# Kernel tuning notes

Measured on AMD Instinct MI355X. Metric: run time of the kernel, lower is better.

Reference implementation:

```python
import jax, jax.numpy as jnp
import numpy as np

N, M, D, C = 8192, 4096, 512, 100


def mish(x):
    return x * jnp.tanh(jax.nn.softplus(x))


def encode_dml(x, W1, b1, W2, b2):
    # two Linear(d_in, d_in) layers each followed by Mish
    h = mish(x @ W1 + b1)
    return mish(h @ W2 + b2)


def setup_inputs() -> dict:
    key = jax.random.key(0)
    ks = jax.random.split(key, 8)
    s = 1.0 / np.sqrt(D)
    x = jax.random.normal(ks[0], (N, D), dtype=jnp.float32)
    samples = jax.random.normal(ks[1], (M, D), dtype=jnp.float32)
    W1 = jax.random.normal(ks[2], (D, D), dtype=jnp.float32) * s
    b1 = jnp.zeros((D,), dtype=jnp.float32)
    W2 = jax.random.normal(ks[3], (D, D), dtype=jnp.float32) * s
    b2 = jnp.zeros((D,), dtype=jnp.float32)
    Wp = jax.random.normal(ks[4], (M, C), dtype=jnp.float32) * (1.0 / np.sqrt(M))
    bp = jnp.zeros((C,), dtype=jnp.float32)
    return {"x": x, "samples": samples, "W1": W1, "b1": b1,
            "W2": W2, "b2": b2, "Wp": Wp, "bp": bp}


def reference(x, samples, W1, b1, W2, b2, Wp, bp):
    xe = encode_dml(x, W1, b1, W2, b2)        # [N, D]
    se = encode_dml(samples, W1, b1, W2, b2)  # [M, D]
    # Euclidean distance to every anchor, GEMM-trick form of
    # torch.norm(x[:,None,:] - s[None,:,:], dim=-1)
    d2 = (jnp.sum(xe * xe, axis=1)[:, None]
          + jnp.sum(se * se, axis=1)[None, :]
          - 2.0 * (xe @ se.T))                # [N, M]
    dist = jnp.sqrt(jnp.maximum(d2, 0.0))
    z = jnp.tanh(dist @ Wp + bp)              # [N, C]
    return jax.nn.log_softmax(z, axis=1)
```

## Files before the change

### kernel.cpp

```cpp
#include <hip/hip_runtime.h>
#include <hip/hip_bf16.h>
#include <math.h>

#define N_ 8192
#define M_ 4096
#define R_ 12288
#define D_ 512
#define C_ 100
#define CP_ 112
#define NSPLIT_ 8
#define MTILES_ ((M_ / NSPLIT_) / 128)

typedef _Float16 f16;
typedef f16  f16x8 __attribute__((ext_vector_type(8)));
typedef f16  f16x4 __attribute__((ext_vector_type(4)));
typedef float f32x4 __attribute__((ext_vector_type(4)));

__device__ __forceinline__ float mishf(float v) {
    float sp = fmaxf(v, 0.f) + log1pf(expf(-fabsf(v)));
    return v * tanhf(sp);
}

__global__ void prep_all(const float* __restrict__ W1, const float* __restrict__ W2,
                         const float* __restrict__ Wp,
                         f16* __restrict__ w1t, f16* __restrict__ w2t,
                         f16* __restrict__ wpT, float* __restrict__ n2) {
    __shared__ char pshm[57856];
    const int bid = blockIdx.x, t = threadIdx.x;
    if (bid < 128) {
        float (*ls)[68] = (float (*)[68])pshm;
        const float* W = (bid < 64) ? W1 : W2;
        f16* WT = (bid < 64) ? w1t : w2t;
        int tile = bid & 63;
        int k0 = (tile >> 3) * 64, c0 = (tile & 7) * 64;
        int r = t >> 4, c4 = (t & 15) * 4;
        #pragma unroll
        for (int l = 0; l < 4; ++l) {
            int row = r + 16 * l;
            float4 v = *reinterpret_cast<const float4*>(&W[(size_t)(k0 + row) * D_ + c0 + c4]);
            ls[row][c4 + 0] = v.x; ls[row][c4 + 1] = v.y;
            ls[row][c4 + 2] = v.z; ls[row][c4 + 3] = v.w;
        }
        __syncthreads();
        #pragma unroll
        for (int l = 0; l < 4; ++l) {
            int c = r + 16 * l;
            f16x4 o;
            #pragma unroll
            for (int j = 0; j < 4; ++j) o[j] = (f16)ls[c4 + j][c];
            *reinterpret_cast<f16x4*>(&WT[(size_t)(c0 + c) * D_ + k0 + c4]) = o;
        }
    } else if (bid < 160) {
        float (*lp)[113] = (float (*)[113])pshm;
        int b = bid - 128;
        int m0 = b * 128;
        for (int id = t; id < 128 * C_; id += 256) {
            int mm = id / C_, c = id - mm * C_;
            lp[mm][c] = Wp[(size_t)(m0 + mm) * C_ + c];
        }
        for (int id = t; id < 128 * (CP_ - C_); id += 256) {
            int mm = id / (CP_ - C_), c = C_ + id % (CP_ - C_);
            lp[mm][c] = 0.f;
        }
        __syncthreads();
        for (int id = t; id < CP_ * 128; id += 256) {
            int c = id >> 7, mm = id & 127;
            wpT[(size_t)c * M_ + m0 + mm] = (f16)lp[mm][c];
        }
    } else {
        int b = bid - 160;
        int base = b * (R_ / 16) + t;
        #pragma unroll
        for (int l = 0; l < (R_ / 16) / 256; ++l)
            n2[base + l * 256] = 0.f;
    }
}

template<bool NORMS, bool F32IN>
__global__ __launch_bounds__(256) void enc_mfma(
        const void* __restrict__ A1, const void* __restrict__ A2,
        const f16* __restrict__ WT,
        const float* __restrict__ b, f16* __restrict__ out,
        float* __restrict__ n2) {
    __shared__ char smem[24576];
    char* xs = smem;
    char* ws = smem + 8192;
    char* os = smem;

    const int t = threadIdx.x;
    const int lane = t & 63;
    const int w  = t >> 6;
    const int wr = w >> 1, wc = w & 1;
    const int lr = lane & 15, lk = lane >> 4;
    const int c0 = blockIdx.x * 128;
    const int n0 = blockIdx.y * 64;

    const int srow = t >> 3;
    const int sj   = t & 7;
    const int csA  = sj ^ (srow & 7);
    const float* Af = nullptr;
    const f16*   Ah = nullptr;
    size_t gA0;
    if constexpr (F32IN) {
        int roff = (n0 < N_) ? n0 : (n0 - N_);
        Af = (const float*)((n0 < N_) ? A1 : A2);
        gA0 = (size_t)(roff + srow) * D_ + csA * 8;
    } else {
        Ah = (const f16*)A1;
        gA0 = (size_t)(n0 + srow) * D_ + csA * 8;
    }
    const size_t gW0 = (size_t)(c0 + srow) * D_ + csA * 8;
    char* lA = xs + t * 16;
    char* lW = ws + t * 16;

    f16x8 ra[2], rw[4];
    f32x4 acc[2][4];
    #pragma unroll
    for (int i = 0; i < 2; ++i)
        #pragma unroll
        for (int j = 0; j < 4; ++j) acc[i][j] = (f32x4){0.f, 0.f, 0.f, 0.f};

    auto loadA = [&](int p, int kn) -> f16x8 {
        if constexpr (F32IN) {
            float4 u0 = *(const float4*)(Af + gA0 + (size_t)p * 32 * D_ + kn);
            float4 u1 = *(const float4*)(Af + gA0 + (size_t)p * 32 * D_ + kn + 4);
            f16x8 o;
            o[0] = (f16)u0.x; o[1] = (f16)u0.y; o[2] = (f16)u0.z; o[3] = (f16)u0.w;
            o[4] = (f16)u1.x; o[5] = (f16)u1.y; o[6] = (f16)u1.z; o[7] = (f16)u1.w;
            return o;
        } else {
            return *(const f16x8*)(Ah + gA0 + (size_t)p * 32 * D_ + kn);
        }
    };

    #pragma unroll
    for (int p = 0; p < 2; ++p) ra[p] = loadA(p, 0);
    #pragma unroll
    for (int p = 0; p < 4; ++p) rw[p] = *(const f16x8*)(WT + gW0 + (size_t)p * 32 * D_);

    for (int kc = 0; kc < 8; ++kc) {
        __syncthreads();
        #pragma unroll
        for (int p = 0; p < 2; ++p) *(f16x8*)(lA + p * 4096) = ra[p];
        #pragma unroll
        for (int p = 0; p < 4; ++p) *(f16x8*)(lW + p * 4096) = rw[p];
        if (kc < 7) {
            int kn = (kc + 1) * 64;
            #pragma unroll
            for (int p = 0; p < 2; ++p) ra[p] = loadA(p, kn);
            #pragma unroll
            for (int p = 0; p < 4; ++p) rw[p] = *(const f16x8*)(WT + gW0 + (size_t)p * 32 * D_ + kn);
        }
        __syncthreads();
        #pragma unroll
        for (int ks = 0; ks < 2; ++ks) {
            const int csw = (ks * 4 + lk) ^ (lr & 7);
            f16x8 af[2], bf[4];
            #pragma unroll
            for (int i = 0; i < 2; ++i)
                af[i] = *(const f16x8*)(xs + (wr * 32 + i * 16 + lr) * 128 + csw * 16);
            #pragma unroll
            for (int j = 0; j < 4; ++j)
                bf[j] = *(const f16x8*)(ws + (wc * 64 + j * 16 + lr) * 128 + csw * 16);
            #pragma unroll
            for (int i = 0; i < 2; ++i)
                #pragma unroll
                for (int j = 0; j < 4; ++j)
                    acc[i][j] = __builtin_amdgcn_mfma_f32_16x16x32_f16(af[i], bf[j], acc[i][j], 0, 0, 0);
        }
    }
    __syncthreads();
    {
        float bv[4];
        #pragma unroll
        for (int j = 0; j < 4; ++j) bv[j] = b[c0 + wc * 64 + j * 16 + lr];
        float rn[2][4] = {};
        #pragma unroll
        for (int i = 0; i < 2; ++i)
            #pragma unroll
            for (int j = 0; j < 4; ++j)
                #pragma unroll
                for (int q = 0; q < 4; ++q) {
                    float v = mishf(acc[i][j][q] + bv[j]);
                    f16 h = (f16)v;
                    int row_l = wr * 32 + i * 16 + lk * 4 + q;
                    int col_l = wc * 64 + j * 16 + lr;
                    *(f16*)(os + row_l * 256 + (((col_l >> 3) ^ (row_l & 7)) * 16) + (col_l & 7) * 2) = h;
                    if (NORMS) { float fv = (float)h; rn[i][q] = fmaf(fv, fv, rn[i][q]); }
                }
        if (NORMS) {
            #pragma unroll
            for (int i = 0; i < 2; ++i)
                #pragma unroll
                for (int q = 0; q < 4; ++q) {
                    float s = rn[i][q];
                    s += __shfl_xor(s, 1, 64); s += __shfl_xor(s, 2, 64);
                    s += __shfl_xor(s, 4, 64); s += __shfl_xor(s, 8, 64);
                    if (lr == 0)
                        atomicAdd(&n2[n0 + wr * 32 + i * 16 + lk * 4 + q], s);
                }
        }
    }
    __syncthreads();
    #pragma unroll
    for (int l2 = 0; l2 < 4; ++l2) {
        int id = t + l2 * 256;
        int row = id >> 4, cc = id & 15;
        f16x8 v = *(const f16x8*)(os + row * 256 + ((cc ^ (row & 7)) * 16));
        *(f16x8*)(out + (size_t)(n0 + row) * D_ + c0 + cc * 8) = v;
    }
}

#define LDA3 72
#define LDD3 136
__global__ __launch_bounds__(256, 2) void fused_mfma(
        const f16* __restrict__ xe, const f16* __restrict__ se,
        const float* __restrict__ xn2, const float* __restrict__ sn2,
        const f16* __restrict__ WpT, f16* __restrict__ zpart) {
    __shared__ char smem[72192];
    f16*   xs = (f16*)smem;
    f16*   ss = (f16*)(smem + 18432);
    f16*   wp = (f16*)smem;
    f16*   ds = (f16*)(smem + 36864);
    float* xn = (float*)(smem + 71680);

    const int t    = threadIdx.x;
    const int lane = t & 63;
    const int w    = t >> 6;
    const int wr   = w >> 1, wc = w & 1;
    const int lr   = lane & 15, lk = lane >> 4;

    const int n0    = blockIdx.x * 128;
    const int mbase = blockIdx.y * (M_ / NSPLIT_);

    if (t < 128) xn[t] = xn2[n0 + t];

    f32x4 zacc[2][7];
    #pragma unroll
    for (int i = 0; i < 2; ++i)
        #pragma unroll
        for (int j = 0; j < 7; ++j)
            zacc[i][j] = (f32x4){0.f, 0.f, 0.f, 0.f};

    for (int mt = 0; mt < MTILES_; ++mt) {
        const int m0 = mbase + mt * 128;
        f32x4 sacc[4][4];
        #pragma unroll
        for (int i = 0; i < 4; ++i)
            #pragma unroll
            for (int j = 0; j < 4; ++j)
                sacc[i][j] = (f32x4){0.f, 0.f, 0.f, 0.f};

        for (int kc = 0; kc < 8; ++kc) {
            __syncthreads();
            {
                int r = t >> 3, ko = (t & 7) * 8;
                int kg = kc * 64 + ko;
                #pragma unroll
                for (int l = 0; l < 4; ++l) {
                    int row = r + 32 * l;
                    *reinterpret_cast<f16x8*>(&xs[row * LDA3 + ko]) =
                        *reinterpret_cast<const f16x8*>(&xe[(size_t)(n0 + row) * D_ + kg]);
                    *reinterpret_cast<f16x8*>(&ss[row * LDA3 + ko]) =
                        *reinterpret_cast<const f16x8*>(&se[(size_t)(m0 + row) * D_ + kg]);
                }
            }
            __syncthreads();
            #pragma unroll
            for (int ks = 0; ks < 2; ++ks) {
                f16x8 af[4], bf[4];
                #pragma unroll
                for (int i = 0; i < 4; ++i) {
                    af[i] = *reinterpret_cast<const f16x8*>(&xs[(wr * 64 + i * 16 + lr) * LDA3 + ks * 32 + lk * 8]);
                    bf[i] = *reinterpret_cast<const f16x8*>(&ss[(wc * 64 + i * 16 + lr) * LDA3 + ks * 32 + lk * 8]);
                }
                #pragma unroll
                for (int i = 0; i < 4; ++i)
                    #pragma unroll
                    for (int j = 0; j < 4; ++j)
                        sacc[i][j] = __builtin_amdgcn_mfma_f32_16x16x32_f16(af[i], bf[j], sacc[i][j], 0, 0, 0);
            }
        }
        {
            float snr[4];
            #pragma unroll
            for (int j = 0; j < 4; ++j) snr[j] = sn2[m0 + wc * 64 + j * 16 + lr];
            #pragma unroll
            for (int i = 0; i < 4; ++i) {
                #pragma unroll
                for (int j = 0; j < 4; ++j) {
                    #pragma unroll
                    for (int q = 0; q < 4; ++q) {
                        int row_l = wr * 64 + i * 16 + lk * 4 + q;
                        int col_l = wc * 64 + j * 16 + lr;
                        float d2 = xn[row_l] + snr[j] - 2.f * sacc[i][j][q];
                        ds[row_l * LDD3 + col_l] = (f16)sqrtf(fmaxf(d2, 0.f));
                    }
                }
            }
        }
        __syncthreads();
        #pragma unroll
        for (int l = 0; l < 7; ++l) {
            int id = t + l * 256;
            int c = id >> 4, mo = (id & 15) * 8;
            *reinterpret_cast<f16x8*>(&wp[c * LDD3 + mo]) =
                *reinterpret_cast<const f16x8*>(&WpT[(size_t)c * M_ + m0 + mo]);
        }
        __syncthreads();
        #pragma unroll
        for (int ks = 0; ks < 4; ++ks) {
            f16x8 aF0 = *reinterpret_cast<const f16x8*>(&ds[(w * 32 + 0  + lr) * LDD3 + ks * 32 + lk * 8]);
            f16x8 aF1 = *reinterpret_cast<const f16x8*>(&ds[(w * 32 + 16 + lr) * LDD3 + ks * 32 + lk * 8]);
            #pragma unroll
            for (int cb = 0; cb < 7; ++cb) {
                f16x8 bF = *reinterpret_cast<const f16x8*>(&wp[(cb * 16 + lr) * LDD3 + ks * 32 + lk * 8]);
                zacc[0][cb] = __builtin_amdgcn_mfma_f32_16x16x32_f16(aF0, bF, zacc[0][cb], 0, 0, 0);
                zacc[1][cb] = __builtin_amdgcn_mfma_f32_16x16x32_f16(aF1, bF, zacc[1][cb], 0, 0, 0);
            }
        }
    }
    #pragma unroll
    for (int ar = 0; ar < 2; ++ar) {
        #pragma unroll
        for (int cb = 0; cb < 7; ++cb) {
            #pragma unroll
            for (int q = 0; q < 4; ++q) {
                int row = n0 + w * 32 + ar * 16 + lk * 4 + q;
                int col = cb * 16 + lr;
                zpart[((size_t)blockIdx.y * N_ + row) * CP_ + col] = (f16)zacc[ar][cb][q];
            }
        }
    }
}

__global__ void z_epilogue(const f16* __restrict__ zpart, const float* __restrict__ bp,
                           float* __restrict__ out) {
    const int w = threadIdx.x >> 6, lane = threadIdx.x & 63;
    const int row = blockIdx.x * 4 + w;
    float z0 = 0.f, z1 = 0.f;
    #pragma unroll
    for (int s = 0; s < NSPLIT_; ++s) {
        const f16* zp = &zpart[((size_t)s * N_ + row) * CP_];
        z0 += (float)zp[lane];
        if (lane + 64 < CP_) z1 += (float)zp[lane + 64];
    }
    float t0 = tanhf(z0 + bp[lane]);
    bool  v1 = (lane + 64) < C_;
    float t1 = v1 ? tanhf(z1 + bp[lane + 64]) : -INFINITY;
    float mx = fmaxf(t0, t1);
    #pragma unroll
    for (int m = 1; m < 64; m <<= 1) mx = fmaxf(mx, __shfl_xor(mx, m, 64));
    float se_ = expf(t0 - mx) + (v1 ? expf(t1 - mx) : 0.f);
    #pragma unroll
    for (int m = 1; m < 64; m <<= 1) se_ += __shfl_xor(se_, m, 64);
    float lse = mx + logf(se_);
    out[(size_t)row * C_ + lane] = t0 - lse;
    if (v1) out[(size_t)row * C_ + lane + 64] = t1 - lse;
}

extern "C" void kernel_launch(void* const* d_in, const int* in_sizes, int n_in,
                              void* d_out, int out_size, void* d_ws, size_t ws_size,
                              hipStream_t stream) {
    const float* x       = (const float*)d_in[0];
    const float* samples = (const float*)d_in[1];
    const float* W1      = (const float*)d_in[2];
    const float* b1      = (const float*)d_in[3];
    const float* W2      = (const float*)d_in[4];
    const float* b2      = (const float*)d_in[5];
    const float* Wp      = (const float*)d_in[6];
    const float* bp      = (const float*)d_in[7];
    float* out = (float*)d_out;

    char* p = (char*)d_ws;
    f16* zpart = (f16*)p;
    f16* h   = (f16*)(p + 12582912);
    f16* w1t = (f16*)(p + 25165824);
    f16* w2t = (f16*)(p + 25690112);
    p += 29360128;
    f16*  ef  = (f16*)p;   p += (size_t)R_ * D_ * 2;
    float* n2  = (float*)p; p += (size_t)R_ * 4;
    f16*  wpT = (f16*)p;   p += (size_t)CP_ * M_ * 2;

    dim3 blk(256);
    prep_all<<<176, blk, 0, stream>>>(W1, W2, Wp, w1t, w2t, wpT, n2);
    enc_mfma<false, true><<<dim3(4, R_ / 64), blk, 0, stream>>>(x, samples, w1t, b1, h, nullptr);
    enc_mfma<true, false><<<dim3(4, R_ / 64), blk, 0, stream>>>(h, nullptr, w2t, b2, ef, n2);
    fused_mfma<<<dim3(N_ / 128, NSPLIT_), blk, 0, stream>>>(ef, ef + (size_t)N_ * D_,
                                                           n2, n2 + N_, wpT, zpart);
    z_epilogue<<<N_ / 4, blk, 0, stream>>>(zpart, bp, out);
}
```

Measured before the change: 169.2 us.

## Double-buffer distance GEMM K-loop with register prefetch in fused_mfma

The xe/se tile loads in the fused distance kernel's K-loop now go through registers into a two-slot shared-memory buffer. The global loads for chunk k+1 are issued before the MFMAs on chunk k and stored to the other slot afterwards, so each K-step needs one barrier instead of two. The second slot overlaps the ds region, so a barrier now sits after the loop instead of before the Wp staging. The minimum-blocks hint in launch_bounds is dropped, which gives the compiler more room for the extra prefetch registers but may lower occupancy.

```diff
diff --git a/kernel.cpp b/kernel.cpp
--- a/kernel.cpp
+++ b/kernel.cpp
@@ -213,16 +213,14 @@
 
 #define LDA3 72
 #define LDD3 136
-__global__ __launch_bounds__(256, 2) void fused_mfma(
+__global__ __launch_bounds__(256) void fused_mfma(
         const f16* __restrict__ xe, const f16* __restrict__ se,
         const float* __restrict__ xn2, const float* __restrict__ sn2,
         const f16* __restrict__ WpT, f16* __restrict__ zpart) {
-    __shared__ char smem[72192];
-    f16*   xs = (f16*)smem;
-    f16*   ss = (f16*)(smem + 18432);
+    __shared__ char smem[74240];
     f16*   wp = (f16*)smem;
     f16*   ds = (f16*)(smem + 36864);
-    float* xn = (float*)(smem + 71680);
+    float* xn = (float*)(smem + 73728);
 
     const int t    = threadIdx.x;
     const int lane = t & 63;
@@ -233,6 +231,9 @@
     const int n0    = blockIdx.x * 128;
     const int mbase = blockIdx.y * (M_ / NSPLIT_);
 
+    const int r_  = t >> 3;
+    const int ko_ = (t & 7) * 8;
+
     if (t < 128) xn[t] = xn2[n0 + t];
 
     f32x4 zacc[2][7];
@@ -251,28 +252,36 @@
             for (int j = 0; j < 4; ++j)
                 sacc[i][j] = (f32x4){0.f, 0.f, 0.f, 0.f};
 
+        __syncthreads();
+        #pragma unroll
+        for (int l = 0; l < 4; ++l) {
+            int row = r_ + 32 * l;
+            *(f16x8*)(smem + (row * LDA3 + ko_) * 2) =
+                *(const f16x8*)(&xe[(size_t)(n0 + row) * D_ + ko_]);
+            *(f16x8*)(smem + 36864  - 36864 + 18432 + (row * LDA3 + ko_) * 2) =
+                *(const f16x8*)(&se[(size_t)(m0 + row) * D_ + ko_]);
+        }
+
+        f16x8 rx[4], rs[4];
         for (int kc = 0; kc < 8; ++kc) {
             __syncthreads();
-            {
-                int r = t >> 3, ko = (t & 7) * 8;
-                int kg = kc * 64 + ko;
+            const int cur = (kc & 1) ? 36864 : 0;
+            if (kc < 7) {
+                const int kg = (kc + 1) * 64 + ko_;
                 #pragma unroll
                 for (int l = 0; l < 4; ++l) {
-                    int row = r + 32 * l;
-                    *reinterpret_cast<f16x8*>(&xs[row * LDA3 + ko]) =
-                        *reinterpret_cast<const f16x8*>(&xe[(size_t)(n0 + row) * D_ + kg]);
-                    *reinterpret_cast<f16x8*>(&ss[row * LDA3 + ko]) =
-                        *reinterpret_cast<const f16x8*>(&se[(size_t)(m0 + row) * D_ + kg]);
-                }
-            }
-            __syncthreads();
+                    int row = r_ + 32 * l;
+                    rx[l] = *(const f16x8*)(&xe[(size_t)(n0 + row) * D_ + kg]);
+                    rs[l] = *(const f16x8*)(&se[(size_t)(m0 + row) * D_ + kg]);
+                }
+            }
             #pragma unroll
             for (int ks = 0; ks < 2; ++ks) {
                 f16x8 af[4], bf[4];
                 #pragma unroll
                 for (int i = 0; i < 4; ++i) {
-                    af[i] = *reinterpret_cast<const f16x8*>(&xs[(wr * 64 + i * 16 + lr) * LDA3 + ks * 32 + lk * 8]);
-                    bf[i] = *reinterpret_cast<const f16x8*>(&ss[(wc * 64 + i * 16 + lr) * LDA3 + ks * 32 + lk * 8]);
+                    af[i] = *(const f16x8*)(smem + cur + ((wr * 64 + i * 16 + lr) * LDA3 + ks * 32 + lk * 8) * 2);
+                    bf[i] = *(const f16x8*)(smem + cur + 18432 + ((wc * 64 + i * 16 + lr) * LDA3 + ks * 32 + lk * 8) * 2);
                 }
                 #pragma unroll
                 for (int i = 0; i < 4; ++i)
@@ -280,7 +289,17 @@
                     for (int j = 0; j < 4; ++j)
                         sacc[i][j] = __builtin_amdgcn_mfma_f32_16x16x32_f16(af[i], bf[j], sacc[i][j], 0, 0, 0);
             }
-        }
+            if (kc < 7) {
+                const int nxt = ((kc + 1) & 1) ? 36864 : 0;
+                #pragma unroll
+                for (int l = 0; l < 4; ++l) {
+                    int row = r_ + 32 * l;
+                    *(f16x8*)(smem + nxt + (row * LDA3 + ko_) * 2) = rx[l];
+                    *(f16x8*)(smem + nxt + 18432 + (row * LDA3 + ko_) * 2) = rs[l];
+                }
+            }
+        }
+        __syncthreads();
         {
             float snr[4];
             #pragma unroll
@@ -299,7 +318,6 @@
                 }
             }
         }
-        __syncthreads();
         #pragma unroll
         for (int l = 0; l < 7; ++l) {
             int id = t + l * 256;
```

Measured after the change: 214.1 us. +26.6%, slower.

## Double-buffer distance-GEMM tiles with direct global-to-LDS loads and XOR swizzle

Applied to the files above, without the earlier changes.

The xe/se tile staging in the fused distance kernel now uses global_load_lds 16-byte transfers into an XOR-swizzled, unpadded layout. The tiles are double-buffered so the next k-chunk's load is issued before the current chunk's MFMAs, which removes one barrier per k iteration. The shared-memory map is rearranged so the distance and Wp tiles reuse the staging buffers. The goal is to overlap global memory latency with matrix math and avoid the register round-trip and padding. Correctness depends on the compiler inserting the vmcnt waits before each barrier.

```diff
diff --git a/kernel.cpp b/kernel.cpp
--- a/kernel.cpp
+++ b/kernel.cpp
@@ -19,6 +19,12 @@
 __device__ __forceinline__ float mishf(float v) {
     float sp = fmaxf(v, 0.f) + log1pf(expf(-fabsf(v)));
     return v * tanhf(sp);
+}
+
+__device__ __forceinline__ void gll16(const void* g, void* l) {
+    __builtin_amdgcn_global_load_lds(
+        (const __attribute__((address_space(1))) unsigned int*)g,
+        (__attribute__((address_space(3))) unsigned int*)l, 16, 0, 0);
 }
 
 __global__ void prep_all(const float* __restrict__ W1, const float* __restrict__ W2,
@@ -211,18 +217,15 @@
     }
 }
 
-#define LDA3 72
 #define LDD3 136
 __global__ __launch_bounds__(256, 2) void fused_mfma(
         const f16* __restrict__ xe, const f16* __restrict__ se,
         const float* __restrict__ xn2, const float* __restrict__ sn2,
         const f16* __restrict__ WpT, f16* __restrict__ zpart) {
-    __shared__ char smem[72192];
-    f16*   xs = (f16*)smem;
-    f16*   ss = (f16*)(smem + 18432);
-    f16*   wp = (f16*)smem;
-    f16*   ds = (f16*)(smem + 36864);
-    float* xn = (float*)(smem + 71680);
+    __shared__ char smem[67840];
+    f16*   ds = (f16*)smem;
+    f16*   wp = (f16*)(smem + 36864);
+    float* xn = (float*)(smem + 67328);
 
     const int t    = threadIdx.x;
     const int lane = t & 63;
@@ -233,6 +236,12 @@
     const int n0    = blockIdx.x * 128;
     const int mbase = blockIdx.y * (M_ / NSPLIT_);
 
+    const int sub  = lane >> 3;
+    const int cswz = (lane & 7) ^ sub;
+    const char* gX = (const char*)(xe + (size_t)(n0 + w * 32 + sub) * D_) + cswz * 16;
+    char* dstX0 = smem + w * 4096;
+    char* dstS0 = smem + 16384 + w * 4096;
+
     if (t < 128) xn[t] = xn2[n0 + t];
 
     f32x4 zacc[2][7];
@@ -244,6 +253,8 @@
 
     for (int mt = 0; mt < MTILES_; ++mt) {
         const int m0 = mbase + mt * 128;
+        const char* gS = (const char*)(se + (size_t)(m0 + w * 32 + sub) * D_) + cswz * 16;
+
         f32x4 sacc[4][4];
         #pragma unroll
         for (int i = 0; i < 4; ++i)
@@ -251,28 +262,33 @@
             for (int j = 0; j < 4; ++j)
                 sacc[i][j] = (f32x4){0.f, 0.f, 0.f, 0.f};
 
+        __syncthreads();
+        #pragma unroll
+        for (int s = 0; s < 4; ++s) {
+            gll16(gX + s * 8192, dstX0 + s * 1024);
+            gll16(gS + s * 8192, dstS0 + s * 1024);
+        }
+
         for (int kc = 0; kc < 8; ++kc) {
             __syncthreads();
-            {
-                int r = t >> 3, ko = (t & 7) * 8;
-                int kg = kc * 64 + ko;
-                #pragma unroll
-                for (int l = 0; l < 4; ++l) {
-                    int row = r + 32 * l;
-                    *reinterpret_cast<f16x8*>(&xs[row * LDA3 + ko]) =
-                        *reinterpret_cast<const f16x8*>(&xe[(size_t)(n0 + row) * D_ + kg]);
-                    *reinterpret_cast<f16x8*>(&ss[row * LDA3 + ko]) =
-                        *reinterpret_cast<const f16x8*>(&se[(size_t)(m0 + row) * D_ + kg]);
+            const int cur = (kc & 1) * 32768;
+            if (kc < 7) {
+                const int nb  = ((kc + 1) & 1) * 32768;
+                const int off = (kc + 1) * 128;
+                #pragma unroll
+                for (int s = 0; s < 4; ++s) {
+                    gll16(gX + off + s * 8192, dstX0 + nb + s * 1024);
+                    gll16(gS + off + s * 8192, dstS0 + nb + s * 1024);
                 }
             }
-            __syncthreads();
             #pragma unroll
             for (int ks = 0; ks < 2; ++ks) {
+                const int csw = (ks * 4 + lk) ^ (lr & 7);
                 f16x8 af[4], bf[4];
                 #pragma unroll
                 for (int i = 0; i < 4; ++i) {
-                    af[i] = *reinterpret_cast<const f16x8*>(&xs[(wr * 64 + i * 16 + lr) * LDA3 + ks * 32 + lk * 8]);
-                    bf[i] = *reinterpret_cast<const f16x8*>(&ss[(wc * 64 + i * 16 + lr) * LDA3 + ks * 32 + lk * 8]);
+                    af[i] = *(const f16x8*)(smem + cur + (wr * 64 + i * 16 + lr) * 128 + csw * 16);
+                    bf[i] = *(const f16x8*)(smem + cur + 16384 + (wc * 64 + i * 16 + lr) * 128 + csw * 16);
                 }
                 #pragma unroll
                 for (int i = 0; i < 4; ++i)
@@ -281,6 +297,7 @@
                         sacc[i][j] = __builtin_amdgcn_mfma_f32_16x16x32_f16(af[i], bf[j], sacc[i][j], 0, 0, 0);
             }
         }
+        __syncthreads();
         {
             float snr[4];
             #pragma unroll
@@ -299,7 +316,6 @@
                 }
             }
         }
-        __syncthreads();
         #pragma unroll
         for (int l = 0; l < 7; ++l) {
             int id = t + l * 256;
```

Result: slower. 186.6 us (+10.3%).
